# Performance work log

Measured on AMD Instinct MI355X. Metric: run time of the kernel, lower is better.

Reference implementation:

```python
import jax, jax.numpy as jnp
import numpy as np

IN_DIM = 256
H_DIM = 256
NUM_NODES = 32768
MAX_NEIGH = 16  # padded neighbor slots; x has 1 + MAX_NEIGH rows per node


def _linear_params(key, fan_in, fan_out):
    kw, kb = jax.random.split(key)
    bound = 1.0 / np.sqrt(fan_in)
    w = jax.random.uniform(kw, (fan_out, fan_in), jnp.float32, -bound, bound)
    b = jax.random.uniform(kb, (fan_out,), jnp.float32, -bound, bound)
    return w, b


def setup_inputs() -> dict:
    key = jax.random.key(0)
    ks = jax.random.split(key, 8)
    x = jax.random.normal(ks[0], (NUM_NODES, 1 + MAX_NEIGH, IN_DIM), jnp.float32)
    # counts[i] in [0, MAX_NEIGH); true neighbor count = counts[i] + 1 (>=1, matches ragged lists)
    counts = jax.random.randint(ks[1], (NUM_NODES,), 0, MAX_NEIGH, jnp.int32)
    Wx_w, Wx_b = _linear_params(ks[2], IN_DIM, H_DIM)
    Wh_w, Wh_b = _linear_params(ks[3], H_DIM, H_DIM)
    Uh_w, Uh_b = _linear_params(ks[4], H_DIM, H_DIM)
    Wg_w, Wg_b = _linear_params(ks[5], H_DIM, H_DIM)
    Ug_w, Ug_b = _linear_params(ks[6], H_DIM, H_DIM)
    return {"x": x, "counts": counts,
            "Wx_w": Wx_w, "Wx_b": Wx_b, "Wh_w": Wh_w, "Wh_b": Wh_b,
            "Uh_w": Uh_w, "Uh_b": Uh_b, "Wg_w": Wg_w, "Wg_b": Wg_b,
            "Ug_w": Ug_w, "Ug_b": Ug_b}


def reference(x, counts, Wx_w, Wx_b, Wh_w, Wh_b, Uh_w, Uh_b, Wg_w, Wg_b, Ug_w, Ug_b):
    # x: [N, 1+K, in_dim]; row 0 = center, rows 1: = (padded) neighbors
    proj = jnp.tanh(jnp.einsum('nkd,hd->nkh', x, Wx_w) + Wx_b)  # [N, 1+K, h]
    center = proj[:, 0, :]            # [N, h]
    neigh = proj[:, 1:, :]            # [N, K, h]
    K = neigh.shape[1]
    n_valid = counts + 1              # true neighbor counts in [1, K]
    mask = jnp.arange(K)[None, :] < n_valid[:, None]  # [N, K]

    # sigmoid(Wh(center) + Uh(neighbors)), per-feature softmax over neighbor axis
    temp = jax.nn.sigmoid((center @ Wh_w.T + Wh_b)[:, None, :]
                          + jnp.einsum('nkh,gh->nkg', neigh, Uh_w) + Uh_b)  # [N, K, h]
    a = jax.nn.softmax(temp, axis=1, where=mask[:, :, None])  # masked slots -> 0 weight
    con = jnp.sum(a * neigh, axis=1)  # [N, h]

    gate = jax.nn.sigmoid(center @ Wg_w.T + Wg_b + con @ Ug_w.T + Ug_b)
    out = gate * center + (1.0 - gate) * con
    # nn.Dropout(0.5) is identity in eval mode; omitted for a deterministic baseline
    return out
```

## Files before the change

kernel.cpp:

```cpp
#include <hip/hip_runtime.h>
#include <hip/hip_bf16.h>
#include <stdint.h>

#define NODES 32768
#define DIM 256
#define ROWS17 17
#define LOG2E 1.4426950408889634f

typedef __attribute__((ext_vector_type(8))) short s16x8;
typedef __attribute__((ext_vector_type(8))) unsigned short u16x8;
typedef __attribute__((ext_vector_type(4))) float f32x4;

__device__ __forceinline__ unsigned short f2bf(float f) {
  union { __hip_bfloat16 h; unsigned short u; } c;
  c.h = __float2bfloat16(f);
  return c.u;
}
__device__ __forceinline__ unsigned int f2bf2(float a, float b) {
  union { __hip_bfloat162 h; unsigned int u; } c;
  c.h = __float22bfloat162_rn(make_float2(a, b));
  return c.u;
}
__device__ __forceinline__ float bf2f(unsigned short h) {
  return __uint_as_float(((unsigned int)h) << 16);
}
__device__ __forceinline__ float fsig(float x) {
  return __builtin_amdgcn_rcpf(1.0f + __builtin_amdgcn_exp2f(-LOG2E * x));
}
__device__ __forceinline__ float ftanh(float x) {
  float e = __builtin_amdgcn_exp2f(x * (2.0f * LOG2E));
  return __builtin_fmaf(-2.0f, __builtin_amdgcn_rcpf(1.0f + e), 1.0f);
}

#define GEMM64B(BMAT, ACC, BIAS)                                               \
  do {                                                                         \
    const s16x8* bp =                                                          \
        (const s16x8*)((BMAT) + ((wv * 32 + l15) * 256 + l4 * 8));             \
    _Pragma("unroll") for (int mt = 0; mt < 4; ++mt)                           \
        _Pragma("unroll") for (int nt = 0; nt < 2; ++nt)                       \
            ACC[mt][nt] = (f32x4)(BIAS[nt]);                                   \
    _Pragma("unroll") for (int ks = 0; ks < 8; ++ks) {                         \
      s16x8 afr[4];                                                            \
      s16x8 bfr[2];                                                            \
      int ab = (l15 * 512 + l4 * 16 + ks * 64) ^ ((l15 & 7) << 4);             \
      _Pragma("unroll") for (int mt = 0; mt < 4; ++mt)                         \
          afr[mt] = *(const s16x8*)(xab + (ab + mt * 8192));                   \
      _Pragma("unroll") for (int nt = 0; nt < 2; ++nt)                         \
          bfr[nt] = bp[nt * 512 + ks * 4];                                     \
      _Pragma("unroll") for (int mt = 0; mt < 4; ++mt)                         \
          _Pragma("unroll") for (int nt = 0; nt < 2; ++nt)                     \
              ACC[mt][nt] = __builtin_amdgcn_mfma_f32_16x16x32_bf16(           \
                  afr[mt], bfr[nt], ACC[mt][nt], 0, 0, 0);                     \
    }                                                                          \
  } while (0)

#define GEMM64D(BM1, BM2, ACC1, ACC2, BI1, BI2)                                \
  do {                                                                         \
    const s16x8* bp1 =                                                         \
        (const s16x8*)((BM1) + ((wv * 32 + l15) * 256 + l4 * 8));              \
    const s16x8* bp2 =                                                         \
        (const s16x8*)((BM2) + ((wv * 32 + l15) * 256 + l4 * 8));              \
    _Pragma("unroll") for (int mt = 0; mt < 4; ++mt)                           \
        _Pragma("unroll") for (int nt = 0; nt < 2; ++nt) {                     \
      ACC1[mt][nt] = (f32x4)(BI1[nt]);                                         \
      ACC2[mt][nt] = (f32x4)(BI2[nt]);                                         \
    }                                                                          \
    _Pragma("unroll") for (int ks = 0; ks < 8; ++ks) {                         \
      s16x8 afr[4];                                                            \
      s16x8 bfr1[2];                                                           \
      s16x8 bfr2[2];                                                           \
      int ab = (l15 * 512 + l4 * 16 + ks * 64) ^ ((l15 & 7) << 4);             \
      _Pragma("unroll") for (int mt = 0; mt < 4; ++mt)                         \
          afr[mt] = *(const s16x8*)(xab + (ab + mt * 8192));                   \
      _Pragma("unroll") for (int nt = 0; nt < 2; ++nt) {                       \
        bfr1[nt] = bp1[nt * 512 + ks * 4];                                     \
        bfr2[nt] = bp2[nt * 512 + ks * 4];                                     \
      }                                                                        \
      _Pragma("unroll") for (int mt = 0; mt < 4; ++mt)                         \
          _Pragma("unroll") for (int nt = 0; nt < 2; ++nt) {                   \
        ACC1[mt][nt] = __builtin_amdgcn_mfma_f32_16x16x32_bf16(                \
            afr[mt], bfr1[nt], ACC1[mt][nt], 0, 0, 0);                         \
        ACC2[mt][nt] = __builtin_amdgcn_mfma_f32_16x16x32_bf16(                \
            afr[mt], bfr2[nt], ACC2[mt][nt], 0, 0, 0);                         \
      }                                                                        \
    }                                                                          \
  } while (0)

__global__ __launch_bounds__(256) void k_cvtw(const float* __restrict__ w0,
                                              const float* __restrict__ w1,
                                              const float* __restrict__ w2,
                                              const float* __restrict__ w3,
                                              const float* __restrict__ w4,
                                              unsigned short* __restrict__ dst,
                                              int* __restrict__ gcnt) {
  if (blockIdx.x == 0 && threadIdx.x < 3) gcnt[threadIdx.x] = 0;
  int idx = (blockIdx.x * 256 + threadIdx.x) * 8;
  int which = idx >> 16;
  int off = idx & 65535;
  const float* src = which == 0 ? w0 : which == 1 ? w1 : which == 2 ? w2
                   : which == 3 ? w3 : w4;
  const f32x4* s4 = (const f32x4*)(src + off);
  f32x4 a = s4[0], b = s4[1];
  u16x8 v;
  unsigned int* vp = (unsigned int*)&v;
  vp[0] = f2bf2(a[0], a[1]);
  vp[1] = f2bf2(a[2], a[3]);
  vp[2] = f2bf2(b[0], b[1]);
  vp[3] = f2bf2(b[2], b[3]);
  *(u16x8*)(dst + idx) = v;
}

__global__ __launch_bounds__(512) void k_sort(const int* __restrict__ counts,
                                              int* __restrict__ perm,
                                              int* __restrict__ gcnt) {
  __shared__ int h[3];
  __shared__ int base[3];
  const int tid = threadIdx.x;
  if (tid < 3) h[tid] = 0;
  __syncthreads();
  int node = blockIdx.x * 512 + tid;
  int nv = counts[node] + 1;
  int b = nv <= 4 ? 0 : nv <= 8 ? 1 : 2;
  int slot = atomicAdd(&h[b], 1);
  __syncthreads();
  if (tid < 3) base[tid] = atomicAdd(&gcnt[tid], h[tid]);
  __syncthreads();
  perm[b * NODES + base[b] + slot] = node;
}

__global__ __launch_bounds__(512) void k_center(
    const float* __restrict__ x, const unsigned short* __restrict__ wxb,
    const unsigned short* __restrict__ whb, const unsigned short* __restrict__ wgb,
    const float* __restrict__ wx_bias, const float* __restrict__ wh_bias,
    const float* __restrict__ wg_bias, unsigned short* __restrict__ cpw,
    unsigned short* __restrict__ hcw, unsigned short* __restrict__ gcw) {
  __shared__ unsigned short XA[64 * 256];
  char* xab = (char*)XA;
  const int tid = threadIdx.x;
  const int lane = tid & 63;
  const int wv = tid >> 6;
  const int l15 = lane & 15;
  const int l4 = lane >> 4;
  const int n0 = blockIdx.x * 64;

#pragma unroll
  for (int i = 0; i < 4; ++i) {
    int chunk = i * 512 + tid;
    int row = chunk >> 5;
    int e0 = (chunk & 31) * 8;
    int node = n0 + row;
    const f32x4* s4 = (const f32x4*)(x + (node * (ROWS17 * DIM) + e0));
    f32x4 f0 = s4[0], f1 = s4[1];
    u16x8 v;
    unsigned int* vp = (unsigned int*)&v;
    vp[0] = f2bf2(f0[0], f0[1]);
    vp[1] = f2bf2(f0[2], f0[3]);
    vp[2] = f2bf2(f1[0], f1[1]);
    vp[3] = f2bf2(f1[2], f1[3]);
    *(u16x8*)(xab + ((row * 512 + e0 * 2) ^ ((row & 7) << 4))) = v;
  }
  __syncthreads();

  float b1[2];
#pragma unroll
  for (int nt = 0; nt < 2; ++nt) b1[nt] = wx_bias[wv * 32 + nt * 16 + l15];
  f32x4 acc[4][2];
  GEMM64B(wxb, acc, b1);
  __syncthreads();

#pragma unroll
  for (int mt = 0; mt < 4; ++mt) {
#pragma unroll
    for (int nt = 0; nt < 2; ++nt) {
      int h = wv * 32 + nt * 16 + l15;
#pragma unroll
      for (int r = 0; r < 4; ++r) {
        int rl = mt * 16 + 4 * l4 + r;
        unsigned short o = f2bf(ftanh(acc[mt][nt][r]));
        *(unsigned short*)(xab + ((rl * 512 + h * 2) ^ ((rl & 7) << 4))) = o;
      }
    }
  }
  __syncthreads();

#pragma unroll
  for (int i = 0; i < 4; ++i) {
    int chunk = i * 512 + tid;
    int row = chunk >> 5;
    int e0 = (chunk & 31) * 8;
    u16x8 v = *(const u16x8*)(xab + ((row * 512 + e0 * 2) ^ ((row & 7) << 4)));
    *(u16x8*)(cpw + ((n0 + row) * 256 + e0)) = v;
  }

  float b2[2], b3[2];
#pragma unroll
  for (int nt = 0; nt < 2; ++nt) {
    b2[nt] = wh_bias[wv * 32 + nt * 16 + l15];
    b3[nt] = wg_bias[wv * 32 + nt * 16 + l15];
  }
  f32x4 acc2[4][2];
  GEMM64D(whb, wgb, acc, acc2, b2, b3);
#pragma unroll
  for (int mt = 0; mt < 4; ++mt)
#pragma unroll
    for (int nt = 0; nt < 2; ++nt) {
      int h = wv * 32 + nt * 16 + l15;
#pragma unroll
      for (int r = 0; r < 4; ++r) {
        int rl = mt * 16 + 4 * l4 + r;
        hcw[(n0 + rl) * 256 + h] = f2bf(acc[mt][nt][r]);
        gcw[(n0 + rl) * 256 + h] = f2bf(acc2[mt][nt][r]);
      }
    }
}

__global__ __launch_bounds__(512, 4) void k_neigh(
    const float* __restrict__ x, const int* __restrict__ counts,
    const unsigned short* __restrict__ wxb, const unsigned short* __restrict__ uhb,
    const float* __restrict__ wx_bias, const float* __restrict__ uh_bias,
    const unsigned short* __restrict__ hcw, unsigned short* __restrict__ conw,
    const int* __restrict__ perm, const int* __restrict__ bcnt) {
  __shared__ unsigned short XA[64 * 256];
  __shared__ unsigned short HC[16 * 256];
  __shared__ int ndl[16];
  __shared__ int nvs[16];
  char* xab = (char*)XA;
  const int tid = threadIdx.x;
  const int lane = tid & 63;
  const int wv = tid >> 6;
  const int l15 = lane & 15;
  const int l4 = lane >> 4;

  int c0 = bcnt[0], c1 = bcnt[1], c2 = bcnt[2];
  int nb0 = (c0 + 15) >> 4, nb1 = (c1 + 7) >> 3, nb2 = (c2 + 3) >> 2;
  int b = blockIdx.x;
  int s, npb, pbase, valid;
  if (b < nb0) {
    s = 2; npb = 16; pbase = b * 16;
    valid = c0 - b * 16; valid = valid > 16 ? 16 : valid;
  } else if (b < nb0 + nb1) {
    s = 3; npb = 8; int bb = b - nb0; pbase = NODES + bb * 8;
    valid = c1 - bb * 8; valid = valid > 8 ? 8 : valid;
  } else if (b < nb0 + nb1 + nb2) {
    s = 4; npb = 4; int bb = b - nb0 - nb1; pbase = 2 * NODES + bb * 4;
    valid = c2 - bb * 4; valid = valid > 4 ? 4 : valid;
  } else {
    return;
  }
  const int mn1 = (1 << s) - 1;

  if (tid < npb) {
    int nd = (tid < valid) ? perm[pbase + tid] : 0;
    ndl[tid] = nd;
    nvs[tid] = (tid < valid) ? counts[nd] + 1 : 0;
  }
  __syncthreads();

  if (tid < npb * 32) {
    int j = tid >> 5;
    int e0 = (tid & 31) * 8;
    if (j < valid)
      *(u16x8*)(HC + j * 256 + e0) = *(const u16x8*)(hcw + (ndl[j] * 256 + e0));
  }

#pragma unroll
  for (int i = 0; i < 4; ++i) {
    int chunk = i * 512 + tid;
    int row = chunk >> 5;
    int e0 = (chunk & 31) * 8;
    int j = row >> s;
    int nrow = row & mn1;
    u16x8 v;
    if (nrow < nvs[j]) {
      const f32x4* s4 =
          (const f32x4*)(x + ((ndl[j] * ROWS17 + 1 + nrow) * DIM + e0));
      f32x4 f0 = s4[0], f1 = s4[1];
      unsigned int* vp = (unsigned int*)&v;
      vp[0] = f2bf2(f0[0], f0[1]);
      vp[1] = f2bf2(f0[2], f0[3]);
      vp[2] = f2bf2(f1[0], f1[1]);
      vp[3] = f2bf2(f1[2], f1[3]);
    } else {
#pragma unroll
      for (int jj = 0; jj < 8; ++jj) v[jj] = 0;
    }
    *(u16x8*)(xab + ((row * 512 + e0 * 2) ^ ((row & 7) << 4))) = v;
  }
  __syncthreads();

  float b1[2];
#pragma unroll
  for (int nt = 0; nt < 2; ++nt) b1[nt] = wx_bias[wv * 32 + nt * 16 + l15];
  f32x4 acc[4][2];
  GEMM64B(wxb, acc, b1);
  __syncthreads();

  float preg[4][2][4];
#pragma unroll
  for (int mt = 0; mt < 4; ++mt) {
#pragma unroll
    for (int nt = 0; nt < 2; ++nt) {
      int h = wv * 32 + nt * 16 + l15;
#pragma unroll
      for (int r = 0; r < 4; ++r) {
        int row = mt * 16 + 4 * l4 + r;
        float t = ftanh(acc[mt][nt][r]);
        preg[mt][nt][r] = t;
        *(unsigned short*)(xab + ((row * 512 + h * 2) ^ ((row & 7) << 4))) =
            f2bf(t);
      }
    }
  }
  __syncthreads();

  float b2[2];
#pragma unroll
  for (int nt = 0; nt < 2; ++nt) b2[nt] = uh_bias[wv * 32 + nt * 16 + l15];
  GEMM64B(uhb, acc, b2);

  const int wmask = (1 << (s - 2)) - 1;
#pragma unroll
  for (int mt = 0; mt < 4; ++mt) {
    int j = (mt * 16 + 4 * l4) >> s;
    int nv = nvs[j];
#pragma unroll
    for (int nt = 0; nt < 2; ++nt) {
      int g = wv * 32 + nt * 16 + l15;
      float base = bf2f(HC[j * 256 + g]);
      float e[4];
#pragma unroll
      for (int r = 0; r < 4; ++r) {
        int k = (4 * l4 + r) & mn1;
        float sg = fsig(acc[mt][nt][r] + base);
        e[r] = (k < nv) ? __builtin_amdgcn_exp2f(LOG2E * sg) : 0.0f;
      }
      float Z = (e[0] + e[1]) + (e[2] + e[3]);
      float num = e[0] * preg[mt][nt][0] + e[1] * preg[mt][nt][1] +
                  e[2] * preg[mt][nt][2] + e[3] * preg[mt][nt][3];
      if (s >= 3) {
        Z += __shfl_xor(Z, 16);
        num += __shfl_xor(num, 16);
      }
      if (s == 4) {
        Z += __shfl_xor(Z, 32);
        num += __shfl_xor(num, 32);
      }
      if ((l4 & wmask) == 0 && j < valid)
        conw[ndl[j] * 256 + g] = f2bf(num * __builtin_amdgcn_rcpf(Z));
    }
  }
}

__global__ __launch_bounds__(512, 4) void k_final(
    const unsigned short* __restrict__ conw, const unsigned short* __restrict__ ugb,
    const float* __restrict__ ug_bias, const unsigned short* __restrict__ cpw,
    const unsigned short* __restrict__ gcw, float* __restrict__ out) {
  __shared__ unsigned short XA[64 * 256];
  char* xab = (char*)XA;
  const int tid = threadIdx.x;
  const int lane = tid & 63;
  const int wv = tid >> 6;
  const int l15 = lane & 15;
  const int l4 = lane >> 4;
  const int n0 = blockIdx.x * 64;

#pragma unroll
  for (int i = 0; i < 4; ++i) {
    int chunk = i * 512 + tid;
    int row = chunk >> 5;
    int e0 = (chunk & 31) * 8;
    u16x8 v = *(const u16x8*)(conw + ((n0 + row) * 256 + e0));
    *(u16x8*)(xab + ((row * 512 + e0 * 2) ^ ((row & 7) << 4))) = v;
  }
  __syncthreads();

  float bg[2];
#pragma unroll
  for (int nt = 0; nt < 2; ++nt) bg[nt] = ug_bias[wv * 32 + nt * 16 + l15];
  f32x4 acc[4][2];
  GEMM64B(ugb, acc, bg);

#pragma unroll
  for (int mt = 0; mt < 4; ++mt)
#pragma unroll
    for (int nt = 0; nt < 2; ++nt) {
      int h = wv * 32 + nt * 16 + l15;
#pragma unroll
      for (int r = 0; r < 4; ++r) {
        int node = n0 + mt * 16 + 4 * l4 + r;
        float gate = fsig(bf2f(gcw[node * 256 + h]) + acc[mt][nt][r]);
        float c = bf2f(cpw[node * 256 + h]);
        float cn = bf2f(conw[node * 256 + h]);
        out[node * 256 + h] = gate * c + (1.0f - gate) * cn;
      }
    }
}

extern "C" void kernel_launch(void* const* d_in, const int* in_sizes, int n_in,
                              void* d_out, int out_size, void* d_ws, size_t ws_size,
                              hipStream_t stream) {
  (void)in_sizes; (void)n_in; (void)out_size; (void)ws_size;
  const float* x = (const float*)d_in[0];
  const int* counts = (const int*)d_in[1];
  const float* Wx_w = (const float*)d_in[2];
  const float* Wx_b = (const float*)d_in[3];
  const float* Wh_w = (const float*)d_in[4];
  const float* Wh_b = (const float*)d_in[5];
  const float* Uh_w = (const float*)d_in[6];
  const float* Uh_b = (const float*)d_in[7];
  const float* Wg_w = (const float*)d_in[8];
  const float* Wg_b = (const float*)d_in[9];
  const float* Ug_w = (const float*)d_in[10];
  const float* Ug_b = (const float*)d_in[11];

  unsigned short* ws = (unsigned short*)d_ws;
  unsigned short* wxb = ws;
  unsigned short* whb = ws + 65536;
  unsigned short* uhb = ws + 131072;
  unsigned short* wgb = ws + 196608;
  unsigned short* ugb = ws + 262144;
  unsigned short* cpw = ws + 327680;
  unsigned short* hcw = cpw + NODES * 256;
  unsigned short* gcw = hcw + NODES * 256;
  unsigned short* conw = gcw + NODES * 256;
  int* perm = (int*)(conw + NODES * 256);
  int* gcnt = perm + 3 * NODES;
  float* out = (float*)d_out;

  hipLaunchKernelGGL(k_cvtw, dim3(160), dim3(256), 0, stream,
                     Wx_w, Wh_w, Uh_w, Wg_w, Ug_w, ws, gcnt);
  hipLaunchKernelGGL(k_sort, dim3(NODES / 512), dim3(512), 0, stream,
                     counts, perm, gcnt);
  hipLaunchKernelGGL(k_center, dim3(NODES / 64), dim3(512), 0, stream,
                     x, wxb, whb, wgb, Wx_b, Wh_b, Wg_b, cpw, hcw, gcw);
  hipLaunchKernelGGL(k_neigh, dim3(NODES / 4 + 3), dim3(512), 0, stream,
                     x, counts, wxb, uhb, Wx_b, Uh_b, hcw, conw, perm, gcnt);
  hipLaunchKernelGGL(k_final, dim3(NODES / 64), dim3(512), 0, stream,
                     conw, ugb, Ug_b, cpw, gcw, out);
}
```

Baseline: 305.7 us.

## Fuse final gating GEMM into neighbor kernel via shared-memory con tile

Result: slower. 413.7 us (+35.3%).

```diff
diff --git a/kernel.cpp b/kernel.cpp
--- a/kernel.cpp
+++ b/kernel.cpp
@@ -217,14 +217,18 @@
 __global__ __launch_bounds__(512, 4) void k_neigh(
     const float* __restrict__ x, const int* __restrict__ counts,
     const unsigned short* __restrict__ wxb, const unsigned short* __restrict__ uhb,
-    const float* __restrict__ wx_bias, const float* __restrict__ uh_bias,
-    const unsigned short* __restrict__ hcw, unsigned short* __restrict__ conw,
+    const unsigned short* __restrict__ ugb, const float* __restrict__ wx_bias,
+    const float* __restrict__ uh_bias, const float* __restrict__ ug_bias,
+    const unsigned short* __restrict__ hcw, const unsigned short* __restrict__ cpw,
+    const unsigned short* __restrict__ gcw, float* __restrict__ out,
     const int* __restrict__ perm, const int* __restrict__ bcnt) {
   __shared__ unsigned short XA[64 * 256];
   __shared__ unsigned short HC[16 * 256];
+  __shared__ unsigned short CN[16 * 256];
   __shared__ int ndl[16];
   __shared__ int nvs[16];
   char* xab = (char*)XA;
+  char* cnb = (char*)CN;
   const int tid = threadIdx.x;
   const int lane = tid & 63;
   const int wv = tid >> 6;
@@ -346,54 +350,47 @@
         num += __shfl_xor(num, 32);
       }
       if ((l4 & wmask) == 0 && j < valid)
-        conw[ndl[j] * 256 + g] = f2bf(num * __builtin_amdgcn_rcpf(Z));
-    }
-  }
-}
-
-__global__ __launch_bounds__(512, 4) void k_final(
-    const unsigned short* __restrict__ conw, const unsigned short* __restrict__ ugb,
-    const float* __restrict__ ug_bias, const unsigned short* __restrict__ cpw,
-    const unsigned short* __restrict__ gcw, float* __restrict__ out) {
-  __shared__ unsigned short XA[64 * 256];
-  char* xab = (char*)XA;
-  const int tid = threadIdx.x;
-  const int lane = tid & 63;
-  const int wv = tid >> 6;
-  const int l15 = lane & 15;
-  const int l4 = lane >> 4;
-  const int n0 = blockIdx.x * 64;
-
-#pragma unroll
-  for (int i = 0; i < 4; ++i) {
-    int chunk = i * 512 + tid;
-    int row = chunk >> 5;
-    int e0 = (chunk & 31) * 8;
-    u16x8 v = *(const u16x8*)(conw + ((n0 + row) * 256 + e0));
-    *(u16x8*)(xab + ((row * 512 + e0 * 2) ^ ((row & 7) << 4))) = v;
+        *(unsigned short*)(cnb + ((j * 512 + g * 2) ^ ((j & 7) << 4))) =
+            f2bf(num * __builtin_amdgcn_rcpf(Z));
+    }
   }
   __syncthreads();
 
   float bg[2];
 #pragma unroll
   for (int nt = 0; nt < 2; ++nt) bg[nt] = ug_bias[wv * 32 + nt * 16 + l15];
-  f32x4 acc[4][2];
-  GEMM64B(ugb, acc, bg);
-
-#pragma unroll
-  for (int mt = 0; mt < 4; ++mt)
-#pragma unroll
-    for (int nt = 0; nt < 2; ++nt) {
-      int h = wv * 32 + nt * 16 + l15;
-#pragma unroll
-      for (int r = 0; r < 4; ++r) {
-        int node = n0 + mt * 16 + 4 * l4 + r;
-        float gate = fsig(bf2f(gcw[node * 256 + h]) + acc[mt][nt][r]);
-        float c = bf2f(cpw[node * 256 + h]);
-        float cn = bf2f(conw[node * 256 + h]);
-        out[node * 256 + h] = gate * c + (1.0f - gate) * cn;
-      }
-    }
+  f32x4 acc3[2];
+  {
+    const s16x8* bp =
+        (const s16x8*)(ugb + ((wv * 32 + l15) * 256 + l4 * 8));
+#pragma unroll
+    for (int nt = 0; nt < 2; ++nt) acc3[nt] = (f32x4)(bg[nt]);
+#pragma unroll
+    for (int ks = 0; ks < 8; ++ks) {
+      s16x8 afr = *(const s16x8*)(
+          cnb + ((l15 * 512 + l4 * 16 + ks * 64) ^ ((l15 & 7) << 4)));
+#pragma unroll
+      for (int nt = 0; nt < 2; ++nt)
+        acc3[nt] = __builtin_amdgcn_mfma_f32_16x16x32_bf16(
+            afr, bp[nt * 512 + ks * 4], acc3[nt], 0, 0, 0);
+    }
+  }
+#pragma unroll
+  for (int nt = 0; nt < 2; ++nt) {
+    int g = wv * 32 + nt * 16 + l15;
+#pragma unroll
+    for (int r = 0; r < 4; ++r) {
+      int nr = 4 * l4 + r;
+      if (nr < valid) {
+        int nd = ndl[nr];
+        float gate = fsig(bf2f(gcw[nd * 256 + g]) + acc3[nt][r]);
+        float cpv = bf2f(cpw[nd * 256 + g]);
+        float cnv = bf2f(*(const unsigned short*)(
+            cnb + ((nr * 512 + g * 2) ^ ((nr & 7) << 4))));
+        out[nd * 256 + g] = gate * cpv + (1.0f - gate) * cnv;
+      }
+    }
+  }
 }
 
 extern "C" void kernel_launch(void* const* d_in, const int* in_sizes, int n_in,
@@ -434,7 +431,6 @@
   hipLaunchKernelGGL(k_center, dim3(NODES / 64), dim3(512), 0, stream,
                      x, wxb, whb, wgb, Wx_b, Wh_b, Wg_b, cpw, hcw, gcw);
   hipLaunchKernelGGL(k_neigh, dim3(NODES / 4 + 3), dim3(512), 0, stream,
-                     x, counts, wxb, uhb, Wx_b, Uh_b, hcw, conw, perm, gcnt);
-  hipLaunchKernelGGL(k_final, dim3(NODES / 64), dim3(512), 0, stream,
-                     conw, ugb, Ug_b, cpw, gcw, out);
-}
+                     x, counts, wxb, uhb, ugb, Wx_b, Uh_b, Ug_b,
+                     hcw, cpw, gcw, out, perm, gcnt);
+}
```
